# Kernel tuning notes

Hardware: AMD Instinct MI355X
Metric: run time of the kernel (lower is better)

The kernel has to match this reference:

```python
import jax, jax.numpy as jnp
import numpy as np

B, T, I, U = 64, 1024, 512, 1024


def ternary_quantize(w):
    # alpha = mean|w|; threshold = 0.7*alpha; map to {-alpha, 0, alpha}
    alpha = jnp.mean(jnp.abs(w))
    thr = 0.7 * alpha
    w_t = jnp.where(jnp.abs(w) < thr, jnp.zeros_like(w), jnp.sign(w))
    return alpha * w_t


def setup_inputs() -> dict:
    key = jax.random.key(0)
    k1, k2, k3 = jax.random.split(key, 3)
    x = jax.random.normal(k1, (B, T, I), dtype=jnp.float32)
    kernel = jax.random.normal(k2, (I, 4 * U), dtype=jnp.float32) * 0.05
    recurrent_kernel = jax.random.normal(k3, (U, 4 * U), dtype=jnp.float32) * 0.05
    # keras unit_forget_bias: zeros except ones on the forget-gate quarter
    bias = jnp.concatenate([jnp.zeros((U,)), jnp.ones((U,)), jnp.zeros((2 * U,))]).astype(jnp.float32)
    return {"x": x, "kernel": kernel, "recurrent_kernel": recurrent_kernel, "bias": bias}


def reference(x, kernel, recurrent_kernel, bias):
    kq = ternary_quantize(kernel)            # [I, 4U]
    rq = ternary_quantize(recurrent_kernel)  # [U, 4U]
    # Precompute input projection for all timesteps (math identical to per-step matmul)
    xz = jnp.einsum('bti,ig->btg', x, kq) + bias  # [B, T, 4U]
    xz_t = jnp.transpose(xz, (1, 0, 2))           # [T, B, 4U]

    def step(carry, zx):
        h, c = carry
        z = zx + h @ rq                            # [B, 4U]
        zi, zf, zg, zo = jnp.split(z, 4, axis=-1)  # keras gate order i, f, c, o
        i = jax.nn.sigmoid(zi)
        f = jax.nn.sigmoid(zf)
        g = jnp.tanh(zg)
        o = jax.nn.sigmoid(zo)
        c_new = f * c + i * g
        h_new = o * jnp.tanh(c_new)
        return (h_new, c_new), h_new

    h0 = jnp.zeros((x.shape[0], U), dtype=x.dtype)
    c0 = jnp.zeros((x.shape[0], U), dtype=x.dtype)
    _, hs = jax.lax.scan(step, (h0, c0), xz_t)     # hs: [T, B, U]
    return jnp.transpose(hs, (1, 0, 2))            # return_sequences=True -> [B, T, U]
```

## Files before the change

### kernel.cpp

```cpp
#include <hip/hip_runtime.h>
#include <hip/hip_bf16.h>


typedef __attribute__((ext_vector_type(8))) __bf16 bf16x8;
typedef __attribute__((ext_vector_type(4))) float f32x4;

#define NWG 256
#define WGT 512
#define T_N 1024

__global__ void absum_kernel(const float* __restrict__ w, int n,
                             double* __restrict__ partial) {
  __shared__ double sd[256];
  double s = 0.0;
  for (int i = blockIdx.x * 256 + threadIdx.x; i < n; i += 256 * 256)
    s += fabs((double)w[i]);
  sd[threadIdx.x] = s;
  __syncthreads();
  for (int k = 128; k > 0; k >>= 1) {
    if (threadIdx.x < k) sd[threadIdx.x] += sd[threadIdx.x + k];
    __syncthreads();
  }
  if (threadIdx.x == 0) partial[blockIdx.x] = sd[0];
}

__global__ void alpha_finalize(const double* __restrict__ pk,
                               const double* __restrict__ pr,
                               float* __restrict__ alphas) {
  __shared__ double sd[256];
  int t = threadIdx.x;
  sd[t] = pk[t];
  __syncthreads();
  for (int s = 128; s > 0; s >>= 1) {
    if (t < s) sd[t] += sd[t + s];
    __syncthreads();
  }
  if (t == 0) alphas[0] = (float)(sd[0] / (512.0 * 4096.0));
  __syncthreads();
  sd[t] = pr[t];
  __syncthreads();
  for (int s = 128; s > 0; s >>= 1) {
    if (t < s) sd[t] += sd[t + s];
    __syncthreads();
  }
  if (t == 0) alphas[1] = (float)(sd[0] / (1024.0 * 4096.0));
}

__global__ void quant_kernel(const float* __restrict__ w, int kbits,
                             const float* __restrict__ alphas, int ai,
                             __hip_bfloat16* __restrict__ wt, int total) {
  int idx = blockIdx.x * 256 + threadIdx.x;
  if (idx >= total) return;
  float thr = 0.7f * alphas[ai];
  int K = 1 << kbits;
  int c = idx >> kbits;
  int k = idx & (K - 1);
  float v = w[k * 4096 + (c & 3) * 1024 + (c >> 2)];
  float q = (fabsf(v) < thr) ? 0.0f : ((v > 0.0f) ? 1.0f : ((v < 0.0f) ? -1.0f : 0.0f));
  wt[idx] = __float2bfloat16(q);
}

__device__ __forceinline__ bf16x8 cvt2(f32x4 a, f32x4 b) {
  bf16x8 r;
  r[0] = (__bf16)a[0]; r[1] = (__bf16)a[1];
  r[2] = (__bf16)a[2]; r[3] = (__bf16)a[3];
  r[4] = (__bf16)b[0]; r[5] = (__bf16)b[1];
  r[6] = (__bf16)b[2]; r[7] = (__bf16)b[3];
  return r;
}
__device__ __forceinline__ void ldf4cc(f32x4* d, const float* p) {
  asm volatile("global_load_dwordx4 %0, %1, off sc0 sc1"
               : "=v"(*d) : "v"(p) : "memory");
}
__device__ __forceinline__ float ldfcc(const float* p) {
  float v;
  asm volatile("global_load_dword %0, %1, off sc0 sc1\n\ts_waitcnt vmcnt(0)"
               : "=v"(v) : "v"(p) : "memory");
  return v;
}
__device__ __forceinline__ void stfcc(float* p, float v) {
  asm volatile("global_store_dword %0, %1, off sc0 sc1" ::"v"(p), "v"(v)
               : "memory");
}
__device__ __forceinline__ float sigm(float z) { return 1.0f / (1.0f + __expf(-z)); }
__device__ __forceinline__ float tanhx(float z) {
  float e = __expf(-2.0f * fabsf(z));
  return __builtin_copysignf((1.0f - e) / (1.0f + e), z);
}

__global__ void __launch_bounds__(WGT, 2)
lstm_persist(const float* __restrict__ bias4, const float* __restrict__ alphas,
             const float* __restrict__ x,
             const __hip_bfloat16* __restrict__ wtk,
             const __hip_bfloat16* __restrict__ wtr,
             float* __restrict__ henc,
             float* __restrict__ out) {
  extern __shared__ char lds[];
  char* lwtk = lds;
  float* lz = (float*)(lds + 131072);
  float* lxz = (float*)(lds + 147968);

  const int tid = threadIdx.x;
  const int wg = blockIdx.x;
  const int lane = tid & 63;
  const int wave = tid >> 6;
  const int r16 = lane & 15;
  const int kb8 = (lane >> 4) << 3;

  const int g = wg >> 5;
  const int u = wg & 31;
  const int rb0 = g << 3;

  for (int it = tid; it < 8192; it += WGT) {
    int c = it >> 6, kk = (it & 63) << 3;
    bf16x8 v = *(const bf16x8*)(wtk + (size_t)(u * 128 + c) * 512 + kk);
    *(bf16x8*)(lwtk + (c << 10) + ((kk << 1) ^ ((c & 7) << 4))) = v;
  }

  const int ks0 = (wave & 3) << 8;
  bf16x8 bw[8][4];
  {
    const __hip_bfloat16* wb =
        wtr + (size_t)(u * 128 + ((wave >> 2) << 6) + r16) * 1024 + ks0 + kb8;
#pragma unroll
    for (int ks = 0; ks < 8; ++ks)
#pragma unroll
      for (int nt = 0; nt < 4; ++nt)
        bw[ks][nt] = *(const bf16x8*)(wb + (size_t)nt * 16 * 1024 + (ks << 5));
  }

  const float ak = alphas[0];
  const float ar = alphas[1];

  const int rl = tid >> 5;
  const int ul = tid & 31;
  float bias_c[4];
#pragma unroll
  for (int gg = 0; gg < 4; ++gg)
    bias_c[gg] = bias4[gg * 1024 + u * 32 + ul];
  float cst = 0.0f;
  float* hstf = henc + (((g << 3) + rl) << 10) + u * 32 + ul;
  float* outp = out + ((size_t)(rb0 + rl) << 20) + u * 32 + ul;

  const float* hldb = henc + ((((g << 3) + (r16 & 7)) << 10)) + ks0 + kb8;
  const float* canp = henc + (((g << 3) + 7) << 10) + ks0 + ((lane & 7) << 5) + 31;

  auto xproj = [&](int tt, int par) {
    const float* xr =
        x + ((size_t)(rb0 + (r16 & 7)) << 19) + ((size_t)tt << 9) + kb8;
    const int cloc = (wave << 4) + r16;
    const char* bbase = lwtk + (cloc << 10);
    const int bxor = (cloc & 7) << 4;
    f32x4 a = {0.f, 0.f, 0.f, 0.f};
#pragma unroll
    for (int kw = 0; kw < 16; ++kw) {
      bf16x8 af = cvt2(*(const f32x4*)(xr + kw * 32),
                       *(const f32x4*)(xr + kw * 32 + 4));
      bf16x8 bf = *(const bf16x8*)(bbase + ((((kw << 5) + kb8) << 1) ^ bxor));
      a = __builtin_amdgcn_mfma_f32_16x16x32_bf16(af, bf, a, 0, 0, 0);
    }
    if (lane < 32) {
      float* dst = lxz + par * 1056 + (wave << 4) + (lane & 15);
#pragma unroll
      for (int j = 0; j < 4; ++j)
        dst[(((lane >> 4) << 2) + j) * 132] = a[j];
    }
  };

  __syncthreads();
  xproj(0, 0);

  for (int t = 0; t < T_N; ++t) {
    {
      f32x4 acc[4];
#pragma unroll
      for (int nt = 0; nt < 4; ++nt) acc[nt] = (f32x4){0.f, 0.f, 0.f, 0.f};
      if (t > 0) {
        const float cexp = (float)(4 * ((t - 1) & 3) + 2);
        const int poff = (t & 1) << 16;
        {
          const float* cp = canp + poff;
          for (;;) {
            float v = (lane < 8) ? ldfcc(cp) : cexp;
            if (__all(fabsf(v - cexp) < 1.002f)) break;
            __builtin_amdgcn_s_sleep(1);
          }
        }
        bf16x8 fr[8];
#pragma unroll
        for (int ks = 0; ks < 8; ++ks)
#pragma unroll
          for (int j = 0; j < 8; ++j) fr[ks][j] = (__bf16)0.0f;
        const float* hb = hldb + poff;
        const f32x4 c4 = {cexp, cexp, cexp, cexp};
#pragma unroll
        for (int half = 0; half < 2; ++half) {
          f32x4 e[8];
          for (;;) {
            if (r16 < 8) {
#pragma unroll
              for (int ks = 0; ks < 4; ++ks) {
                ldf4cc(&e[2 * ks], hb + (((half << 2) + ks) << 5));
                ldf4cc(&e[2 * ks + 1], hb + (((half << 2) + ks) << 5) + 4);
              }
              asm volatile("s_waitcnt vmcnt(0)" ::: "memory");
            }
            float dev = 0.0f;
            if (r16 < 8) {
#pragma unroll
              for (int i = 0; i < 8; ++i)
#pragma unroll
                for (int j = 0; j < 4; ++j)
                  dev = fmaxf(dev, fabsf(e[i][j] - cexp));
            }
            if (__all(dev < 1.002f)) break;
            __builtin_amdgcn_s_sleep(1);
          }
          if (r16 < 8) {
#pragma unroll
            for (int ks = 0; ks < 4; ++ks)
              fr[(half << 2) + ks] = cvt2(e[2 * ks] - c4, e[2 * ks + 1] - c4);
          }
        }
        __builtin_amdgcn_sched_barrier(0);
#pragma unroll
        for (int ks = 0; ks < 8; ++ks)
#pragma unroll
          for (int nt = 0; nt < 4; ++nt)
            acc[nt] = __builtin_amdgcn_mfma_f32_16x16x32_bf16(
                fr[ks], bw[ks][nt], acc[nt], 0, 0, 0);
      }
      if (lane < 32) {
        float* dst = lz + (wave & 3) * 1056 + ((wave >> 2) << 6) + (lane & 15);
#pragma unroll
        for (int nt = 0; nt < 4; ++nt)
#pragma unroll
          for (int j = 0; j < 4; ++j)
            dst[(((lane >> 4) << 2) + j) * 132 + (nt << 4)] = acc[nt][j];
      }
    }
    __syncthreads();

    if (tid < 256) {
      f32x4 z0 = *(const f32x4*)(lz + 0 * 1056 + rl * 132 + (ul << 2));
      f32x4 z1 = *(const f32x4*)(lz + 1 * 1056 + rl * 132 + (ul << 2));
      f32x4 z2 = *(const f32x4*)(lz + 2 * 1056 + rl * 132 + (ul << 2));
      f32x4 z3 = *(const f32x4*)(lz + 3 * 1056 + rl * 132 + (ul << 2));
      f32x4 z = z0 + z1 + z2 + z3;
      f32x4 xv = *(const f32x4*)(lxz + (t & 1) * 1056 + rl * 132 + (ul << 2));
      float zi = ak * xv[0] + bias_c[0] + ar * z[0];
      float zf = ak * xv[1] + bias_c[1] + ar * z[1];
      float zg = ak * xv[2] + bias_c[2] + ar * z[2];
      float zo = ak * xv[3] + bias_c[3] + ar * z[3];
      float ig = sigm(zi), fg = sigm(zf), gg = tanhx(zg), og = sigm(zo);
      float cn = fg * cst + ig * gg;
      cst = cn;
      float ho = og * tanhx(cn);
      float cw = (float)(4 * (t & 3) + 2);
      stfcc(hstf + (((t + 1) & 1) << 16), cw + ho);
      outp[(size_t)t << 10] = ho;
    }
    __syncthreads();

    if (t != T_N - 1) xproj(t + 1, (t + 1) & 1);
  }
}

extern "C" void kernel_launch(void* const* d_in, const int* in_sizes, int n_in,
                              void* d_out, int out_size, void* d_ws, size_t ws_size,
                              hipStream_t stream) {
  const float* x = (const float*)d_in[0];
  const float* wk = (const float*)d_in[1];
  const float* wr = (const float*)d_in[2];
  const float* bs = (const float*)d_in[3];
  float* out = (float*)d_out;
  char* ws = (char*)d_ws;

  float* alphas = (float*)(ws + 0);
  double* pk = (double*)(ws + 1024);
  double* pr = (double*)(ws + 8192);
  __hip_bfloat16* wtk = (__hip_bfloat16*)(ws + 16384);
  __hip_bfloat16* wtr = (__hip_bfloat16*)(ws + 16384 + (4 << 20));
  float* henc = (float*)(ws + 16384 + (12 << 20));

  absum_kernel<<<256, 256, 0, stream>>>(wk, 512 * 4096, pk);
  absum_kernel<<<256, 256, 0, stream>>>(wr, 1024 * 4096, pr);
  alpha_finalize<<<1, 256, 0, stream>>>(pk, pr, alphas);
  quant_kernel<<<(4096 * 512) / 256, 256, 0, stream>>>(wk, 9, alphas, 0, wtk,
                                                       4096 * 512);
  quant_kernel<<<(4096 * 1024) / 256, 256, 0, stream>>>(wr, 10, alphas, 1, wtr,
                                                        4096 * 1024);
  (void)hipMemsetAsync(henc, 0, 2 * 8 * 8 * 1024 * 4);

  const int smem = 131072 + 16896 + 8448;
  (void)hipFuncSetAttribute((const void*)lstm_persist,
                            hipFuncAttributeMaxDynamicSharedMemorySize, smem);
  void* args[] = {(void*)&bs,  (void*)&alphas, (void*)&x, (void*)&wtk,
                  (void*)&wtr, (void*)&henc,   (void*)&out};
  (void)hipLaunchCooperativeKernel((void*)lstm_persist, dim3(NWG), dim3(WGT),
                                   args, smem, stream);
}
```

Measured before the change: 11.94 ms.

## Merge h-poll into one pass, drop canary poll and trailing barrier, remap workgroups

Replaces the canary-then-two-half spin-wait with a single poll over all 16 h vectors. That poll both validates the step tag and supplies the MFMA operands, removing a dependent global round trip per step. It also drops the end-of-step __syncthreads and swaps the workgroup-to-(batch group, unit slice) mapping so that neighbouring workgroup ids cover different batch groups. Removing the barrier relies on the global h polling alone to keep LDS buffers (lz, lxz) from being overwritten early, which could race. Holding more registers live during the poll may also raise register pressure.

```diff
diff --git a/kernel.cpp b/kernel.cpp
--- a/kernel.cpp
+++ b/kernel.cpp
@@ -72,12 +72,6 @@
   asm volatile("global_load_dwordx4 %0, %1, off sc0 sc1"
                : "=v"(*d) : "v"(p) : "memory");
 }
-__device__ __forceinline__ float ldfcc(const float* p) {
-  float v;
-  asm volatile("global_load_dword %0, %1, off sc0 sc1\n\ts_waitcnt vmcnt(0)"
-               : "=v"(v) : "v"(p) : "memory");
-  return v;
-}
 __device__ __forceinline__ void stfcc(float* p, float v) {
   asm volatile("global_store_dword %0, %1, off sc0 sc1" ::"v"(p), "v"(v)
                : "memory");
@@ -107,8 +101,8 @@
   const int r16 = lane & 15;
   const int kb8 = (lane >> 4) << 3;
 
-  const int g = wg >> 5;
-  const int u = wg & 31;
+  const int g = wg & 7;
+  const int u = wg >> 3;
   const int rb0 = g << 3;
 
   for (int it = tid; it < 8192; it += WGT) {
@@ -143,7 +137,6 @@
   float* outp = out + ((size_t)(rb0 + rl) << 20) + u * 32 + ul;
 
   const float* hldb = henc + ((((g << 3) + (r16 & 7)) << 10)) + ks0 + kb8;
-  const float* canp = henc + (((g << 3) + 7) << 10) + ks0 + ((lane & 7) << 5) + 31;
 
   auto xproj = [&](int tt, int par) {
     const float* xr =
@@ -177,50 +170,39 @@
       for (int nt = 0; nt < 4; ++nt) acc[nt] = (f32x4){0.f, 0.f, 0.f, 0.f};
       if (t > 0) {
         const float cexp = (float)(4 * ((t - 1) & 3) + 2);
-        const int poff = (t & 1) << 16;
-        {
-          const float* cp = canp + poff;
-          for (;;) {
-            float v = (lane < 8) ? ldfcc(cp) : cexp;
-            if (__all(fabsf(v - cexp) < 1.002f)) break;
-            __builtin_amdgcn_s_sleep(1);
+        const float* hb = hldb + ((t & 1) << 16);
+        f32x4 e[16];
+        for (;;) {
+          if (r16 < 8) {
+#pragma unroll
+            for (int ks = 0; ks < 8; ++ks) {
+              ldf4cc(&e[2 * ks], hb + (ks << 5));
+              ldf4cc(&e[2 * ks + 1], hb + (ks << 5) + 4);
+            }
+            asm volatile("s_waitcnt vmcnt(0)" ::: "memory");
           }
+          float dev = 0.0f;
+          if (r16 < 8) {
+#pragma unroll
+            for (int i = 0; i < 16; ++i)
+#pragma unroll
+              for (int j = 0; j < 4; ++j)
+                dev = fmaxf(dev, fabsf(e[i][j] - cexp));
+          }
+          if (__all(dev < 1.002f)) break;
+          __builtin_amdgcn_s_sleep(1);
         }
         bf16x8 fr[8];
-#pragma unroll
-        for (int ks = 0; ks < 8; ++ks)
-#pragma unroll
-          for (int j = 0; j < 8; ++j) fr[ks][j] = (__bf16)0.0f;
-        const float* hb = hldb + poff;
-        const f32x4 c4 = {cexp, cexp, cexp, cexp};
-#pragma unroll
-        for (int half = 0; half < 2; ++half) {
-          f32x4 e[8];
-          for (;;) {
-            if (r16 < 8) {
-#pragma unroll
-              for (int ks = 0; ks < 4; ++ks) {
-                ldf4cc(&e[2 * ks], hb + (((half << 2) + ks) << 5));
-                ldf4cc(&e[2 * ks + 1], hb + (((half << 2) + ks) << 5) + 4);
-              }
-              asm volatile("s_waitcnt vmcnt(0)" ::: "memory");
-            }
-            float dev = 0.0f;
-            if (r16 < 8) {
-#pragma unroll
-              for (int i = 0; i < 8; ++i)
-#pragma unroll
-                for (int j = 0; j < 4; ++j)
-                  dev = fmaxf(dev, fabsf(e[i][j] - cexp));
-            }
-            if (__all(dev < 1.002f)) break;
-            __builtin_amdgcn_s_sleep(1);
-          }
-          if (r16 < 8) {
-#pragma unroll
-            for (int ks = 0; ks < 4; ++ks)
-              fr[(half << 2) + ks] = cvt2(e[2 * ks] - c4, e[2 * ks + 1] - c4);
-          }
+        if (r16 < 8) {
+          const f32x4 c4 = {cexp, cexp, cexp, cexp};
+#pragma unroll
+          for (int ks = 0; ks < 8; ++ks)
+            fr[ks] = cvt2(e[2 * ks] - c4, e[2 * ks + 1] - c4);
+        } else {
+#pragma unroll
+          for (int ks = 0; ks < 8; ++ks)
+#pragma unroll
+            for (int j = 0; j < 8; ++j) fr[ks][j] = (__bf16)0.0f;
         }
         __builtin_amdgcn_sched_barrier(0);
 #pragma unroll
@@ -260,7 +242,6 @@
       stfcc(hstf + (((t + 1) & 1) << 16), cw + ho);
       outp[(size_t)t << 10] = ho;
     }
-    __syncthreads();
 
     if (t != T_N - 1) xproj(t + 1, (t + 1) & 1);
   }
```

New measurement: 16.14 ms. +35.2%, slower.
